# Optimization experiments

Measured on AMD Instinct MI355X. Metric: run time of the kernel, lower is better.

Reference implementation:

```python
import jax, jax.numpy as jnp
import numpy as np

# static config (matches init_kwargs)
PL, LAT, LON = 8, 48, 96
WP, WL, WW = 2, 6, 12
SP, SL, SN = 1, 3, 6
NH = 16


def _earth_position_index(ws):
    wp, wl, ww = ws
    zi = np.arange(wp); zj = -np.arange(wp) * wp
    hi = np.arange(wl); hj = -np.arange(wl) * wl
    w = np.arange(ww)
    c1 = np.stack(np.meshgrid(zi, hi, w, indexing='ij')).reshape(3, -1)
    c2 = np.stack(np.meshgrid(zj, hj, w, indexing='ij')).reshape(3, -1)
    coords = (c1[:, :, None] - c2[:, None, :]).transpose(1, 2, 0).astype(np.int64)
    coords[:, :, 2] += ww - 1
    coords[:, :, 1] *= 2 * ww - 1
    coords[:, :, 0] *= (2 * ww - 1) * wl * wl
    return coords.sum(-1)  # (N, N)

_POS_IDX = jnp.asarray(_earth_position_index((WP, WL, WW)))


def _ln(x, w, b, eps=1e-5):
    m = x.mean(-1, keepdims=True)
    v = x.var(-1, keepdims=True)
    return (x - m) / jnp.sqrt(v + eps) * w + b


def setup_inputs() -> dict:
    key = jax.random.key(0)
    ks = jax.random.split(key, 8)
    B, C = 1, 512
    L = PL * LAT * LON
    TOW = (PL // WP) * (LAT // WL)
    TBL = WP * WP * WL * WL * (2 * WW - 1)
    s = 0.02
    return {
        'x': jax.random.normal(ks[0], (B, L, C), jnp.float32),
        'norm1_w': jnp.ones((C,), jnp.float32), 'norm1_b': jnp.zeros((C,), jnp.float32),
        'qkv_w': jax.random.normal(ks[1], (C, 3 * C), jnp.float32) * s,
        'qkv_b': jnp.zeros((3 * C,), jnp.float32),
        'proj_w': jax.random.normal(ks[2], (C, C), jnp.float32) * s,
        'proj_b': jnp.zeros((C,), jnp.float32),
        'bias_table': jax.random.normal(ks[3], (TBL, TOW, NH), jnp.float32) * s,
        'norm2_w': jnp.ones((C,), jnp.float32), 'norm2_b': jnp.zeros((C,), jnp.float32),
        'mlp_w1': jax.random.normal(ks[4], (C, 4 * C), jnp.float32) * s,
        'mlp_b1': jnp.zeros((4 * C,), jnp.float32),
        'mlp_w2': jax.random.normal(ks[5], (4 * C, C), jnp.float32) * s,
        'mlp_b2': jnp.zeros((C,), jnp.float32),
    }


def reference(x, norm1_w, norm1_b, qkv_w, qkv_b, proj_w, proj_b, bias_table,
              norm2_w, norm2_b, mlp_w1, mlp_b1, mlp_w2, mlp_b2):
    B, L, C = x.shape
    HD = C // NH
    scale = HD ** -0.5
    N = WP * WL * WW
    nPl, nLat, nLon = PL // WP, LAT // WL, LON // WW
    nW = nPl * nLat

    # norm1 + roll + window partition (B, nLon, nPl, nLat, wp, wl, ww, C)
    h = _ln(x, norm1_w, norm1_b).reshape(B, PL, LAT, LON, C)
    h = jnp.roll(h, (-SP, -SL, -SN), axis=(1, 2, 3))
    h = h.reshape(B, nPl, WP, nLat, WL, nLon, WW, C)
    h = h.transpose(0, 5, 1, 3, 2, 4, 6, 7).reshape(B * nLon, nW, N, C)

    # attention
    qkv = (h @ qkv_w + qkv_b).reshape(B * nLon, nW, N, 3, NH, HD)
    qkv = qkv.transpose(3, 0, 4, 1, 2, 5)  # (3, B_, nh, nW, N, hd)
    q, k, v = qkv[0] * scale, qkv[1], qkv[2]
    attn = jnp.einsum('bhwnd,bhwmd->bhwnm', q, k)
    bias = bias_table[_POS_IDX.reshape(-1)].reshape(N, N, nW, NH)
    bias = bias.transpose(3, 2, 0, 1)  # (nh, nW, N, N)
    attn = jax.nn.softmax(attn + bias[None], axis=-1)
    o = jnp.einsum('bhwnm,bhwmd->bhwnd', attn, v)
    o = o.transpose(0, 2, 3, 1, 4).reshape(B * nLon, nW, N, C)
    o = o @ proj_w + proj_b

    # reverse partition + roll back
    o = o.reshape(B, nLon, nPl, nLat, WP, WL, WW, C)
    o = o.transpose(0, 2, 4, 3, 5, 1, 6, 7).reshape(B, PL, LAT, LON, C)
    o = jnp.roll(o, (SP, SL, SN), axis=(1, 2, 3)).reshape(B, L, C)

    x = x + o
    h2 = _ln(x, norm2_w, norm2_b)
    h2 = jax.nn.gelu(h2 @ mlp_w1 + mlp_b1, approximate=False) @ mlp_w2 + mlp_b2
    return x + h2
```

## Files before the change

### kernel.cpp

```cpp
#include <hip/hip_runtime.h>
#include <hip/hip_bf16.h>
#include <math.h>

typedef __bf16 bf16;
typedef __attribute__((ext_vector_type(8))) __bf16 bf16x8;
typedef __attribute__((ext_vector_type(4))) float f32x4;
typedef __attribute__((ext_vector_type(8))) float f32x8;

#define NTOK   36864
#define CDIM   512
#define NHEAD  16
#define HD     32
#define NWIN   32
#define NLON   8
#define WTOK   144
#define TBL    3312

#define GLOAD_LDS16(g, l) __builtin_amdgcn_global_load_lds( \
    (const __attribute__((address_space(1))) void*)(const void*)(g), \
    (__attribute__((address_space(3))) void*)(l), 16, 0, 0)

__device__ __forceinline__ int src_token(int r) {
    int ww_ = r % 12; int q = r / 12;
    int wl_ = q % 6;  q /= 6;
    int wp_ = q & 1;  q >>= 1;
    int lat_g = q & 7; q >>= 3;
    int pl_g = q & 3;  q >>= 2;
    int lon_g = q;
    int pl  = pl_g * 2 + wp_ + 1;  if (pl  >= 8)  pl  -= 8;
    int lat = lat_g * 6 + wl_ + 3; if (lat >= 48) lat -= 48;
    int lon = lon_g * 12 + ww_ + 6; if (lon >= 96) lon -= 96;
    return (pl * 48 + lat) * 96 + lon;
}

__device__ __forceinline__ float gelu_exact(float x) {
    return 0.5f * x * (1.0f + erff(x * 0.70710678118654752f));
}

__global__ __launch_bounds__(256) void transpose_weights(const float* __restrict__ qkv_w,
                                                         const float* __restrict__ proj_w,
                                                         const float* __restrict__ w1,
                                                         const float* __restrict__ w2,
                                                         bf16* __restrict__ wtq,
                                                         bf16* __restrict__ wtp,
                                                         bf16* __restrict__ wt1,
                                                         bf16* __restrict__ wt2) {
    __shared__ bf16 tile[32][33];
    int bid = blockIdx.x;
    const float* in; bf16* outp; int R, Cc, ti;
    if (bid < 768)       { in = qkv_w;  outp = wtq; R = 512;  Cc = 1536; ti = bid; }
    else if (bid < 1024) { in = proj_w; outp = wtp; R = 512;  Cc = 512;  ti = bid - 768; }
    else if (bid < 2048) { in = w1;     outp = wt1; R = 512;  Cc = 2048; ti = bid - 1024; }
    else                 { in = w2;     outp = wt2; R = 2048; Cc = 512;  ti = bid - 2048; }
    int gx = Cc >> 5;
    int c0 = (ti % gx) * 32, r0 = (ti / gx) * 32;
    int tx = threadIdx.x & 31, ty = threadIdx.x >> 5;
#pragma unroll
    for (int i = 0; i < 32; i += 8)
        tile[ty + i][tx] = (bf16)in[(size_t)(r0 + ty + i) * Cc + c0 + tx];
    __syncthreads();
#pragma unroll
    for (int i = 0; i < 32; i += 8)
        outp[(size_t)(c0 + ty + i) * R + r0 + tx] = tile[tx][ty + i];
}

__global__ __launch_bounds__(256) void table_transpose(const float* __restrict__ in,
                                                       float* __restrict__ outT) {
    __shared__ float tile[32][33];
    int i0 = blockIdx.x * 32, w0 = blockIdx.y * 32;
    int tx = threadIdx.x & 31, ty = threadIdx.x >> 5;
#pragma unroll
    for (int r = 0; r < 32; r += 8)
        if (i0 + ty + r < TBL) tile[ty + r][tx] = in[(size_t)(i0 + ty + r) * 512 + w0 + tx];
    __syncthreads();
#pragma unroll
    for (int r = 0; r < 32; r += 8)
        if (i0 + tx < TBL) outT[(size_t)(w0 + ty + r) * TBL + i0 + tx] = tile[tx][ty + r];
}

template<bool PERM>
__global__ __launch_bounds__(256) void ln_kernel(const float* __restrict__ in,
                                                 const float* __restrict__ w,
                                                 const float* __restrict__ b,
                                                 bf16* __restrict__ out) {
    int r = blockIdx.x * 4 + (threadIdx.x >> 6);
    int lane = threadIdx.x & 63;
    int s = PERM ? src_token(r) : r;
    f32x8 v8 = *(const f32x8*)(in + (size_t)s * CDIM + lane * 8);
    float sum = 0.f, sq = 0.f;
#pragma unroll
    for (int i = 0; i < 8; ++i) { sum += v8[i]; sq += v8[i] * v8[i]; }
#pragma unroll
    for (int m = 1; m < 64; m <<= 1) { sum += __shfl_xor(sum, m); sq += __shfl_xor(sq, m); }
    float mean = sum * (1.f / 512.f);
    float var  = sq  * (1.f / 512.f) - mean * mean;
    float rstd = rsqrtf(var + 1e-5f);
    f32x8 w8 = *(const f32x8*)(w + lane * 8);
    f32x8 b8 = *(const f32x8*)(b + lane * 8);
    bf16x8 o8;
#pragma unroll
    for (int i = 0; i < 8; ++i)
        o8[i] = (bf16)((v8[i] - mean) * rstd * w8[i] + b8[i]);
    *(bf16x8*)(out + (size_t)r * CDIM + lane * 8) = o8;
}

template<int EPI>
__global__ __launch_bounds__(256) void gemm_bt(const bf16* __restrict__ A,
                                               const bf16* __restrict__ Bt,
                                               const float* __restrict__ bias,
                                               void* __restrict__ Cout_,
                                               const float* __restrict__ X,
                                               int K, int N, int gx) {
    __shared__ bf16 As[2 * 128 * 32];
    __shared__ bf16 Bs[2 * 128 * 32];
    int t = threadIdx.x;
    int wid = t >> 6, lane = t & 63;
    int wr = wid >> 1, wc = wid & 1;
    int g = lane >> 4, cl = lane & 15;

    int nwg = gridDim.x, orig = blockIdx.x;
    int wg = orig;
    if ((nwg & 7) == 0) {
        int cpx = nwg >> 3;
        wg = (orig & 7) * cpx + (orig >> 3);
    }
    int m0 = (wg / gx) * 128, n0 = (wg % gx) * 128;
    f32x4 acc[4][4] = {};

    int srow = wid * 16 + (lane >> 2);
    int scol = (lane & 3) * 8;
    const bf16* Ag0 = A  + (size_t)(m0 + srow) * K + scol;
    const bf16* Ag1 = Ag0 + (size_t)64 * K;
    const bf16* Bg0 = Bt + (size_t)(n0 + srow) * K + scol;
    const bf16* Bg1 = Bg0 + (size_t)64 * K;
    int ldsoff = wid * 16 * 32;

    GLOAD_LDS16(Ag0, As + ldsoff);
    GLOAD_LDS16(Ag1, As + 64 * 32 + ldsoff);
    GLOAD_LDS16(Bg0, Bs + ldsoff);
    GLOAD_LDS16(Bg1, Bs + 64 * 32 + ldsoff);
    __syncthreads();

    int nt = K >> 5, cur = 0;
    for (int kt = 0; kt < nt; ++kt) {
        if (kt + 1 < nt) {
            int k1 = (kt + 1) << 5;
            bf16* Ad = As + (cur ^ 1) * 4096;
            bf16* Bd = Bs + (cur ^ 1) * 4096;
            GLOAD_LDS16(Ag0 + k1, Ad + ldsoff);
            GLOAD_LDS16(Ag1 + k1, Ad + 64 * 32 + ldsoff);
            GLOAD_LDS16(Bg0 + k1, Bd + ldsoff);
            GLOAD_LDS16(Bg1 + k1, Bd + 64 * 32 + ldsoff);
        }
        const bf16* Ar = As + cur * 4096;
        const bf16* Br = Bs + cur * 4096;
        bf16x8 af[4], bfv[4];
#pragma unroll
        for (int i = 0; i < 4; ++i)
            af[i]  = *(const bf16x8*)(Ar + (wr * 64 + i * 16 + cl) * 32 + g * 8);
#pragma unroll
        for (int i = 0; i < 4; ++i)
            bfv[i] = *(const bf16x8*)(Br + (wc * 64 + i * 16 + cl) * 32 + g * 8);
#pragma unroll
        for (int mi = 0; mi < 4; ++mi)
#pragma unroll
            for (int ni = 0; ni < 4; ++ni)
                acc[mi][ni] = __builtin_amdgcn_mfma_f32_16x16x32_bf16(af[mi], bfv[ni], acc[mi][ni], 0, 0, 0);
        __syncthreads();
        cur ^= 1;
    }

#pragma unroll
    for (int mi = 0; mi < 4; ++mi) {
#pragma unroll
        for (int j = 0; j < 4; ++j) {
            int row = m0 + wr * 64 + mi * 16 + g * 4 + j;
            int srw = 0;
            if (EPI == 2) srw = src_token(row);
#pragma unroll
            for (int ni = 0; ni < 4; ++ni) {
                int col = n0 + wc * 64 + ni * 16 + cl;
                float v = acc[mi][ni][j] + bias[col];
                if (EPI == 2) {
                    size_t o = (size_t)srw * CDIM + col;
                    ((float*)Cout_)[o] = X[o] + v;
                } else {
                    size_t o = (size_t)row * N + col;
                    ((float*)Cout_)[o] += v;
                }
            }
        }
    }
}

template<int EPI>
__global__ __launch_bounds__(512, 2) void gemm256(const bf16* __restrict__ A,
                                                  const bf16* __restrict__ Bt,
                                                  const float* __restrict__ bias,
                                                  bf16* __restrict__ Cout,
                                                  int K, int N, int gx) {
    __shared__ char lds[3 * 32768];
    const int t = threadIdx.x;
    const int wid = t >> 6, lane = t & 63;
    const int wr = wid >> 2, wc = wid & 3;
    const int g = lane >> 4, cl = lane & 15;

    int nwg = gridDim.x, orig = blockIdx.x;
    int cpx = nwg >> 3;
    int wg = (orig & 7) * cpx + (orig >> 3);
    const int m0 = (wg / gx) * 256, n0 = (wg % gx) * 256;

    f32x4 acc[8][4] = {};

    const bf16* sbase = (wid < 4) ? A : Bt;
    const int soff0 = (wid < 4) ? m0 : n0;
    const int fr0 = (wid & 3) * 4;
    const int adst = (wid >= 4) ? 16384 : 0;

#define STAGE256(kt, buf) do {                                                        \
        int kk = (kt) << 5;                                                           \
        char* bb = lds + (buf) * 32768 + adst;                                        \
        _Pragma("unroll")                                                             \
        for (int c = 0; c < 4; ++c) {                                                 \
            const bf16* src = sbase + (size_t)(soff0 + (fr0 + c) * 16 + cl) * K + kk + g * 8; \
            GLOAD_LDS16(src, bb + (fr0 + c) * 1024);                                  \
        }                                                                             \
    } while (0)

    const int nt = K >> 5;
    STAGE256(0, 0);
    STAGE256(1, 1);
    asm volatile("s_waitcnt vmcnt(4)" ::: "memory");
    __builtin_amdgcn_s_barrier();

    for (int kt = 0; kt < nt; ++kt) {
        const char* rb = lds + (kt % 3) * 32768;
        bf16x8 aF[4], bF[4];

#pragma unroll
        for (int j = 0; j < 4; ++j)
            aF[j] = *(const bf16x8*)(rb + (wr * 8 + j) * 1024 + lane * 16);
#pragma unroll
        for (int i = 0; i < 4; ++i)
            bF[i] = *(const bf16x8*)(rb + 16384 + (wc * 4 + i) * 1024 + lane * 16);
        if (kt + 2 < nt) STAGE256(kt + 2, (kt + 2) % 3);
        __builtin_amdgcn_s_barrier();
        __builtin_amdgcn_s_setprio(1);
#pragma unroll
        for (int j = 0; j < 4; ++j)
#pragma unroll
            for (int i = 0; i < 4; ++i)
                acc[j][i] = __builtin_amdgcn_mfma_f32_16x16x32_bf16(aF[j], bF[i], acc[j][i], 0, 0, 0);
        __builtin_amdgcn_s_setprio(0);
        __builtin_amdgcn_s_barrier();

#pragma unroll
        for (int j = 0; j < 4; ++j)
            aF[j] = *(const bf16x8*)(rb + (wr * 8 + 4 + j) * 1024 + lane * 16);
        if (kt + 2 < nt)      asm volatile("s_waitcnt vmcnt(4)" ::: "memory");
        else if (kt + 1 < nt) asm volatile("s_waitcnt vmcnt(0)" ::: "memory");
        __builtin_amdgcn_s_barrier();
        __builtin_amdgcn_s_setprio(1);
#pragma unroll
        for (int j = 0; j < 4; ++j)
#pragma unroll
            for (int i = 0; i < 4; ++i)
                acc[4 + j][i] = __builtin_amdgcn_mfma_f32_16x16x32_bf16(aF[j], bF[i], acc[4 + j][i], 0, 0, 0);
        __builtin_amdgcn_s_setprio(0);
        __builtin_amdgcn_s_barrier();
    }
#undef STAGE256

#pragma unroll
    for (int mf = 0; mf < 8; ++mf) {
#pragma unroll
        for (int jj = 0; jj < 4; ++jj) {
            int row = m0 + wr * 128 + mf * 16 + g * 4 + jj;
#pragma unroll
            for (int nf = 0; nf < 4; ++nf) {
                int col = n0 + wc * 64 + nf * 16 + cl;
                float v = acc[mf][nf][jj] + bias[col];
                if (EPI == 1) v = gelu_exact(v);
                Cout[(size_t)row * N + col] = (bf16)v;
            }
        }
    }
}

__global__ __launch_bounds__(256) void attn_mfma(const bf16* __restrict__ qkv,
                                                 const float* __restrict__ tableT,
                                                 bf16* __restrict__ obuf) {
    int wgs = (blockIdx.x & 7) * 512 + (blockIdx.x >> 3);
    int h  = wgs & 15;
    int w  = (wgs >> 4) & 31;
    int b_ = wgs >> 9;
    int t = threadIdx.x, wid = t >> 6, lane = t & 63;
    int g = lane >> 4, cl = lane & 15;
    size_t base = ((size_t)b_ * NWIN + w) * WTOK;

    __shared__ bf16 P[WTOK * 168];
    __shared__ bf16 vT[32 * 168];
    __shared__ float bias_s[TBL];
    bf16* qs = P;
    bf16* ks = P + WTOK * 40;

    const bf16* qg = qkv + base * 1536 + h * 32;
    for (int tok = t >> 2; tok < WTOK; tok += 64) {
        int c8 = (t & 3) * 8;
        *(bf16x8*)(qs + tok * 40 + c8) = *(const bf16x8*)(qg + (size_t)tok * 1536 + c8);
        *(bf16x8*)(ks + tok * 40 + c8) = *(const bf16x8*)(qg + 512 + (size_t)tok * 1536 + c8);
        bf16x8 v8 = *(const bf16x8*)(qg + 1024 + (size_t)tok * 1536 + c8);
#pragma unroll
        for (int i = 0; i < 8; ++i) vT[(c8 + i) * 168 + tok] = v8[i];
    }
    for (int z = t; z < 32 * 24; z += 256) vT[(z / 24) * 168 + 144 + (z % 24)] = (bf16)0.f;
    const float* tb = tableT + (size_t)(w * 16 + h) * TBL;
    for (int i = t; i < TBL; i += 256) bias_s[i] = tb[i];
    __syncthreads();

    f32x4 sacc[3][9] = {};
    bf16x8 kf[9];
#pragma unroll
    for (int ct = 0; ct < 9; ++ct)
        kf[ct] = *(const bf16x8*)(ks + (ct * 16 + cl) * 40 + g * 8);
#pragma unroll
    for (int rti = 0; rti < 3; ++rti) {
        int rt = wid + rti * 4;
        if (rt < 9) {
            bf16x8 qf = *(const bf16x8*)(qs + (rt * 16 + cl) * 40 + g * 8);
#pragma unroll
            for (int ct = 0; ct < 9; ++ct)
                sacc[rti][ct] = __builtin_amdgcn_mfma_f32_16x16x32_bf16(qf, kf[ct], sacc[rti][ct], 0, 0, 0);
        }
    }
    __syncthreads();

    for (int z = t; z < WTOK * 24; z += 256) P[(z / 24) * 168 + 144 + (z % 24)] = (bf16)0.f;

    int bm[9];
#pragma unroll
    for (int ct = 0; ct < 9; ++ct) {
        int m = ct * 16 + cl;
        int wm = m % 12, tm = m / 12, hm = tm % 6, zm = tm / 6;
        bm[ct] = zm * 1656 + hm * 138 + 11 - wm;
    }

    const float scale = 0.17677669529663689f;
    float rinv[3][4];
#pragma unroll
    for (int rti = 0; rti < 3; ++rti) {
        int rt = wid + rti * 4;
        if (rt < 9) {
#pragma unroll
            for (int j = 0; j < 4; ++j) {
                int row = rt * 16 + g * 4 + j;
                int wn = row % 12, tn = row / 12, hn = tn % 6, zn = tn / 6;
                int an = zn * 828 + hn * 23 + wn;
                float mx = -1e30f;
#pragma unroll
                for (int ct = 0; ct < 9; ++ct) {
                    float v = sacc[rti][ct][j] * scale + bias_s[an + bm[ct]];
                    sacc[rti][ct][j] = v;
                    mx = fmaxf(mx, v);
                }
                for (int msk = 1; msk < 16; msk <<= 1) mx = fmaxf(mx, __shfl_xor(mx, msk));
                float sm = 0.f;
#pragma unroll
                for (int ct = 0; ct < 9; ++ct) {
                    float p = __expf(sacc[rti][ct][j] - mx);
                    sm += p;
                    P[row * 168 + ct * 16 + cl] = (bf16)p;
                }
                for (int msk = 1; msk < 16; msk <<= 1) sm += __shfl_xor(sm, msk);
                rinv[rti][j] = 1.f / sm;
            }
        }
    }
    __syncthreads();

#pragma unroll
    for (int rti = 0; rti < 3; ++rti) {
        int rt = wid + rti * 4;
        if (rt < 9) {
            f32x4 oacc[2] = {};
#pragma unroll
            for (int ks_ = 0; ks_ < 5; ++ks_) {
                bf16x8 pf = *(const bf16x8*)(P + (rt * 16 + cl) * 168 + ks_ * 32 + g * 8);
#pragma unroll
                for (int c2 = 0; c2 < 2; ++c2) {
                    bf16x8 vf = *(const bf16x8*)(vT + (c2 * 16 + cl) * 168 + ks_ * 32 + g * 8);
                    oacc[c2] = __builtin_amdgcn_mfma_f32_16x16x32_bf16(pf, vf, oacc[c2], 0, 0, 0);
                }
            }
#pragma unroll
            for (int c2 = 0; c2 < 2; ++c2)
#pragma unroll
                for (int j = 0; j < 4; ++j) {
                    int row = rt * 16 + g * 4 + j;
                    obuf[(base + row) * CDIM + h * 32 + c2 * 16 + cl] =
                        (bf16)(oacc[c2][j] * rinv[rti][j]);
                }
        }
    }
}

extern "C" void kernel_launch(void* const* d_in, const int* in_sizes, int n_in,
                              void* d_out, int out_size, void* d_ws, size_t ws_size,
                              hipStream_t stream) {
    const float* x       = (const float*)d_in[0];
    const float* n1w     = (const float*)d_in[1];
    const float* n1b     = (const float*)d_in[2];
    const float* qkv_w   = (const float*)d_in[3];
    const float* qkv_b   = (const float*)d_in[4];
    const float* proj_w  = (const float*)d_in[5];
    const float* proj_b  = (const float*)d_in[6];
    const float* btab    = (const float*)d_in[7];
    const float* n2w     = (const float*)d_in[8];
    const float* n2b     = (const float*)d_in[9];
    const float* mlp_w1  = (const float*)d_in[10];
    const float* mlp_b1  = (const float*)d_in[11];
    const float* mlp_w2  = (const float*)d_in[12];
    const float* mlp_b2  = (const float*)d_in[13];
    float* out = (float*)d_out;

    const size_t OFF_HBUF = 0;
    const size_t OFF_QKV  = 37748736;
    const size_t OFF_TT   = 150994944;
    const size_t OFF_OBUF = 188743680;
    const size_t OFF_WTQ  = 226492416;
    const size_t OFF_WTP  = 228065280;
    const size_t OFF_WT1  = 228589568;
    const size_t OFF_WT2  = 230686720;
    const size_t NEED     = 232783872;

    if (ws_size < NEED) return;

    char* ws = (char*)d_ws;
    bf16*  hbuf   = (bf16*)(ws + OFF_HBUF);
    bf16*  qkvbuf = (bf16*)(ws + OFF_QKV);
    bf16*  midbuf = qkvbuf;
    float* tableT = (float*)(ws + OFF_TT);
    bf16*  obuf   = (bf16*)(ws + OFF_OBUF);
    bf16*  wtq    = (bf16*)(ws + OFF_WTQ);
    bf16*  wtp    = (bf16*)(ws + OFF_WTP);
    bf16*  wt1    = (bf16*)(ws + OFF_WT1);
    bf16*  wt2    = (bf16*)(ws + OFF_WT2);

    transpose_weights<<<3072, 256, 0, stream>>>(qkv_w, proj_w, mlp_w1, mlp_w2,
                                                wtq, wtp, wt1, wt2);
    table_transpose<<<dim3((TBL + 31) / 32, 512 / 32), 256, 0, stream>>>(btab, tableT);

    ln_kernel<true><<<NTOK / 4, 256, 0, stream>>>(x, n1w, n1b, hbuf);

    gemm256<0><<<144 * 6, 512, 0, stream>>>(hbuf, wtq, qkv_b, qkvbuf, 512, 1536, 6);

    attn_mfma<<<4096, 256, 0, stream>>>(qkvbuf, tableT, obuf);

    gemm_bt<2><<<4 * 288, 256, 0, stream>>>(obuf, wtp, proj_b, out, x, 512, 512, 4);

    ln_kernel<false><<<NTOK / 4, 256, 0, stream>>>(out, n2w, n2b, hbuf);

    gemm256<1><<<144 * 8, 512, 0, stream>>>(hbuf, wt1, mlp_b1, midbuf, 512, 2048, 8);

    gemm_bt<3><<<4 * 288, 256, 0, stream>>>(midbuf, wt2, mlp_b2, out, nullptr, 2048, 512, 4);
}
```

Measured before the change: 604.7 us.

## Deepen gemm256 LDS pipeline to four stages with swizzled row-major tiles

The 256x256 GEMM moves from a 3-stage to a 4-stage LDS ring buffer, prefetching three K-tiles ahead with matching vmcnt waits. Staging now writes row-major 64-byte rows with an XOR swizzle, and fragment reads apply the same swizzle to avoid LDS bank conflicts. Launch bounds drop to one block per SM to fit 128KB of LDS, trading occupancy for deeper latency hiding. gemm_bt also gains bf16/GELU epilogue variants, all instantiated and kept alive.

```diff
diff --git a/kernel.cpp b/kernel.cpp
--- a/kernel.cpp
+++ b/kernel.cpp
@@ -19,6 +19,8 @@
 #define GLOAD_LDS16(g, l) __builtin_amdgcn_global_load_lds( \
     (const __attribute__((address_space(1))) void*)(const void*)(g), \
     (__attribute__((address_space(3))) void*)(l), 16, 0, 0)
+
+#define SWZ(o) ((o) ^ ((((o) >> 7) & 3) << 4))
 
 __device__ __forceinline__ int src_token(int r) {
     int ww_ = r % 12; int q = r / 12;
@@ -181,7 +183,10 @@
             for (int ni = 0; ni < 4; ++ni) {
                 int col = n0 + wc * 64 + ni * 16 + cl;
                 float v = acc[mi][ni][j] + bias[col];
-                if (EPI == 2) {
+                if (EPI == 1) v = gelu_exact(v);
+                if (EPI == 0 || EPI == 1) {
+                    ((bf16*)Cout_)[(size_t)row * N + col] = (bf16)v;
+                } else if (EPI == 2) {
                     size_t o = (size_t)srw * CDIM + col;
                     ((float*)Cout_)[o] = X[o] + v;
                 } else {
@@ -193,13 +198,16 @@
     }
 }
 
+static void* const _keep_gemm_bt[] = {
+    (void*)gemm_bt<0>, (void*)gemm_bt<1>, (void*)gemm_bt<2>, (void*)gemm_bt<3>};
+
 template<int EPI>
-__global__ __launch_bounds__(512, 2) void gemm256(const bf16* __restrict__ A,
+__global__ __launch_bounds__(512, 1) void gemm256(const bf16* __restrict__ A,
                                                   const bf16* __restrict__ Bt,
                                                   const float* __restrict__ bias,
                                                   bf16* __restrict__ Cout,
                                                   int K, int N, int gx) {
-    __shared__ char lds[3 * 32768];
+    __shared__ char lds[4 * 32768];
     const int t = threadIdx.x;
     const int wid = t >> 6, lane = t & 63;
     const int wr = wid >> 2, wc = wid & 3;
@@ -212,38 +220,42 @@
 
     f32x4 acc[8][4] = {};
 
-    const bf16* sbase = (wid < 4) ? A : Bt;
-    const int soff0 = (wid < 4) ? m0 : n0;
-    const int fr0 = (wid & 3) * 4;
-    const int adst = (wid >= 4) ? 16384 : 0;
-
-#define STAGE256(kt, buf) do {                                                        \
-        int kk = (kt) << 5;                                                           \
-        char* bb = lds + (buf) * 32768 + adst;                                        \
-        _Pragma("unroll")                                                             \
-        for (int c = 0; c < 4; ++c) {                                                 \
-            const bf16* src = sbase + (size_t)(soff0 + (fr0 + c) * 16 + cl) * K + kk + g * 8; \
-            GLOAD_LDS16(src, bb + (fr0 + c) * 1024);                                  \
-        }                                                                             \
+    int el = lane ^ ((lane >> 3) & 3);
+    int srow = el >> 2, scol = (el & 3) * 8;
+    const bf16* Ag0 = A  + (size_t)(m0 + wid * 16 + srow) * K + scol;
+    const bf16* Ag1 = Ag0 + (size_t)128 * K;
+    const bf16* Bg0 = Bt + (size_t)(n0 + wid * 16 + srow) * K + scol;
+    const bf16* Bg1 = Bg0 + (size_t)128 * K;
+    const int wb = wid << 10;
+
+#define STAGE256(kt, buf) do {                         \
+        int kk = (kt) << 5;                            \
+        char* bb = lds + (buf) * 32768;                \
+        GLOAD_LDS16(Ag0 + kk, bb + wb);                \
+        GLOAD_LDS16(Ag1 + kk, bb + 8192  + wb);        \
+        GLOAD_LDS16(Bg0 + kk, bb + 16384 + wb);        \
+        GLOAD_LDS16(Bg1 + kk, bb + 24576 + wb);        \
     } while (0)
 
     const int nt = K >> 5;
     STAGE256(0, 0);
     STAGE256(1, 1);
-    asm volatile("s_waitcnt vmcnt(4)" ::: "memory");
+    STAGE256(2, 2);
+    asm volatile("s_waitcnt vmcnt(8)" ::: "memory");
     __builtin_amdgcn_s_barrier();
 
     for (int kt = 0; kt < nt; ++kt) {
-        const char* rb = lds + (kt % 3) * 32768;
+        const char* Ab = lds + (kt & 3) * 32768;
+        const char* Bb = Ab + 16384;
         bf16x8 aF[4], bF[4];
 
 #pragma unroll
         for (int j = 0; j < 4; ++j)
-            aF[j] = *(const bf16x8*)(rb + (wr * 8 + j) * 1024 + lane * 16);
+            aF[j] = *(const bf16x8*)(Ab + SWZ((wr * 128 + j * 16 + cl) * 64 + g * 16));
 #pragma unroll
         for (int i = 0; i < 4; ++i)
-            bF[i] = *(const bf16x8*)(rb + 16384 + (wc * 4 + i) * 1024 + lane * 16);
-        if (kt + 2 < nt) STAGE256(kt + 2, (kt + 2) % 3);
+            bF[i] = *(const bf16x8*)(Bb + SWZ((wc * 64 + i * 16 + cl) * 64 + g * 16));
+        if (kt + 3 < nt) STAGE256(kt + 3, (kt + 3) & 3);
         __builtin_amdgcn_s_barrier();
         __builtin_amdgcn_s_setprio(1);
 #pragma unroll
@@ -256,8 +268,9 @@
 
 #pragma unroll
         for (int j = 0; j < 4; ++j)
-            aF[j] = *(const bf16x8*)(rb + (wr * 8 + 4 + j) * 1024 + lane * 16);
-        if (kt + 2 < nt)      asm volatile("s_waitcnt vmcnt(4)" ::: "memory");
+            aF[j] = *(const bf16x8*)(Ab + SWZ((wr * 128 + (4 + j) * 16 + cl) * 64 + g * 16));
+        if (kt + 3 < nt)      asm volatile("s_waitcnt vmcnt(8)" ::: "memory");
+        else if (kt + 2 < nt) asm volatile("s_waitcnt vmcnt(4)" ::: "memory");
         else if (kt + 1 < nt) asm volatile("s_waitcnt vmcnt(0)" ::: "memory");
         __builtin_amdgcn_s_barrier();
         __builtin_amdgcn_s_setprio(1);
@@ -407,6 +420,7 @@
 extern "C" void kernel_launch(void* const* d_in, const int* in_sizes, int n_in,
                               void* d_out, int out_size, void* d_ws, size_t ws_size,
                               hipStream_t stream) {
+    (void)_keep_gemm_bt;
     const float* x       = (const float*)d_in[0];
     const float* n1w     = (const float*)d_in[1];
     const float* n1b     = (const float*)d_in[2];
```

Result: no change. 598.9 us (-1.0%).
